# Performance work log

Measured on AMD Instinct MI355X. Metric: run time of the kernel, lower is better.

The kernel has to match this reference:

```python
import jax, jax.numpy as jnp
import numpy as np

B, LQ, LK, D = 32, 1024, 1024, 256

def setup_inputs() -> dict:
    key = jax.random.key(0)
    ks = jax.random.split(key, 7)
    return {
        "raw_query": jax.random.normal(ks[0], (B, LQ, D), dtype=jnp.float32),
        "raw_key": jax.random.normal(ks[1], (B, LK, D), dtype=jnp.float32),
        "raw_value": jax.random.normal(ks[2], (B, LK, D), dtype=jnp.float32),
        "value_mask": jax.random.randint(ks[3], (B, LQ), 0, 2, dtype=jnp.int32),
        "WQ": jax.random.normal(ks[4], (D, D), dtype=jnp.float32) * 0.05,
        "WK": jax.random.normal(ks[5], (D, D), dtype=jnp.float32) * 0.05,
        "WV": jax.random.normal(ks[6], (D, D), dtype=jnp.float32) * 0.05,
    }

def reference(raw_query, raw_key, raw_value, value_mask, WQ, WK, WV):
    # Projections: [B, L, D] @ [D, D]
    Q = raw_query @ WQ
    K = raw_key @ WK
    V = raw_value @ WV
    # Scores: [B, LQ, LK] (use_scale=False -> no 1/sqrt(d_k))
    att = jnp.einsum("bqd,bkd->bqk", Q, K)
    # Mask expanded on axis=2 -> zeroes entire query rows of scores (faithful to tf.where+zeros_like)
    att = jnp.where(value_mask[:, :, None] > 0, att, jnp.zeros((), dtype=att.dtype))
    att = jax.nn.softmax(att, axis=-1)
    # Output: [B, LQ, D]
    return jnp.einsum("bqk,bkd->bqd", att, V)
```

## Files before the change

kernel.cpp:

```cpp
#include <hip/hip_runtime.h>
#include <hip/hip_bf16.h>
#include <math.h>

#define B_ 32
#define L_ 1024
#define D_ 256

typedef _Float16 half8 __attribute__((ext_vector_type(8)));
typedef __fp16   fp16x2 __attribute__((ext_vector_type(2)));
typedef short    s16x8 __attribute__((ext_vector_type(8)));
typedef float    f32x4 __attribute__((ext_vector_type(4)));

typedef __attribute__((address_space(3))) unsigned int lds_u32;
typedef __attribute__((address_space(1))) unsigned int gbl_u32;

__device__ __forceinline__ void gl_lds16(const void* g, void* l) {
    __builtin_amdgcn_global_load_lds((gbl_u32*)g, (lds_u32*)l, 16, 0, 0);
}

__device__ __forceinline__ unsigned short f2bf(float x) {
    unsigned u = __float_as_uint(x);
    u += 0x7FFFu + ((u >> 16) & 1u);
    return (unsigned short)(u >> 16);
}

__device__ __forceinline__ unsigned short f2h(float x) {
    _Float16 h = (_Float16)x;
    unsigned short u;
    __builtin_memcpy(&u, &h, 2);
    return u;
}

__device__ __forceinline__ unsigned pkrtz(float a, float b) {
    fp16x2 v = __builtin_amdgcn_cvt_pkrtz(a, b);
    unsigned u;
    __builtin_memcpy(&u, &v, 4);
    return u;
}

__global__ __launch_bounds__(256) void wprep_kernel(
    const float* __restrict__ W0, const float* __restrict__ W1,
    const float* __restrict__ W2, unsigned short* __restrict__ Wt)
{
    const int z = blockIdx.z;
    const float* __restrict__ W = (z == 0) ? W0 : (z == 1) ? W1 : W2;
    __shared__ unsigned short T[64][72];
    const int k0 = blockIdx.x << 6, n0 = blockIdx.y << 6;
    const int t = threadIdx.x;
    const int r = t >> 2, c0 = (t & 3) << 4;
    #pragma unroll
    for (int j = 0; j < 16; j += 4) {
        float4 w4 = *(const float4*)(W + (size_t)(k0 + r) * 256 + n0 + c0 + j);
        T[c0 + j + 0][r] = f2h(w4.x);
        T[c0 + j + 1][r] = f2h(w4.y);
        T[c0 + j + 2][r] = f2h(w4.z);
        T[c0 + j + 3][r] = f2h(w4.w);
    }
    __syncthreads();
    const int n = t >> 2, kc = (t & 3) << 4;
    unsigned short* dst = Wt + ((size_t)z << 16) + (size_t)(n0 + n) * 256 + k0 + kc;
    *(uint4*)(dst + 0) = *(const uint4*)&T[n][kc + 0];
    *(uint4*)(dst + 8) = *(const uint4*)&T[n][kc + 8];
}

__global__ __launch_bounds__(256) void proj_mfma_kernel(
    const float* __restrict__ A0, const float* __restrict__ A1,
    const float* __restrict__ A2, const unsigned short* __restrict__ Wt,
    unsigned short* __restrict__ Qh, unsigned short* __restrict__ Kh,
    unsigned short* __restrict__ Vt)
{
    __shared__ unsigned short SMEM[32768];
    unsigned short* Asm = SMEM;
    unsigned short* Bsm = SMEM + 16384;

    const int z = blockIdx.z;
    const float* __restrict__ A = (z == 0) ? A0 : (z == 1) ? A1 : A2;
    const int bm = blockIdx.x << 7, bn = blockIdx.y << 7;
    const int t = threadIdx.x, lane = t & 63, w = t >> 6;
    const int wm = (w >> 1) << 6, wn = (w & 1) << 6;

    const float* __restrict__ Ag = A + (size_t)bm * 256;
    const unsigned short* __restrict__ Bg = Wt + ((size_t)z << 16) + (size_t)bn * 256;

    f32x4 acc[4][4];
    const f32x4 z4 = {0.f, 0.f, 0.f, 0.f};
    #pragma unroll
    for (int mi = 0; mi < 4; ++mi)
        #pragma unroll
        for (int ni = 0; ni < 4; ++ni) acc[mi][ni] = z4;

    float4 a_reg[8];

    auto loadA = [&](int it) {
        #pragma unroll
        for (int i = 0; i < 8; ++i) {
            int r  = (t >> 4) + (i << 4);
            int c4 = t & 15;
            a_reg[i] = *(const float4*)(Ag + (size_t)r * 256 + (it << 6) + (c4 << 2));
        }
    };
    auto writeA = [&](int buf) {
        #pragma unroll
        for (int i = 0; i < 8; ++i) {
            int r  = (t >> 4) + (i << 4);
            int c4 = t & 15;
            unsigned h01 = pkrtz(a_reg[i].x, a_reg[i].y);
            unsigned h23 = pkrtz(a_reg[i].z, a_reg[i].w);
            int cs = (c4 >> 1) ^ (r & 7);
            uint2 d2; d2.x = h01; d2.y = h23;
            *(uint2*)&Asm[(buf << 13) + (r << 6) + (cs << 3) + ((c4 & 1) << 2)] = d2;
        }
    };
    auto stageB = [&](int buf, int it) {
        #pragma unroll
        for (int rr = 0; rr < 4; ++rr) {
            int o = (rr << 8) + t;
            int r = o >> 3, c = o & 7;
            int cs = c ^ (r & 7);
            gl_lds16(Bg + (size_t)r * 256 + (it << 6) + (cs << 3),
                     &Bsm[(buf << 13) + (o << 3)]);
        }
    };
    auto compute = [&](int buf) {
        #pragma unroll
        for (int kc = 0; kc < 2; ++kc) {
            half8 af[4], bfr[4];
            #pragma unroll
            for (int mi = 0; mi < 4; ++mi) {
                int m = wm + (mi << 4) + (lane & 15);
                int cs = ((kc << 2) + (lane >> 4)) ^ (m & 7);
                af[mi] = *(const half8*)&Asm[(buf << 13) + (m << 6) + (cs << 3)];
            }
            #pragma unroll
            for (int ni = 0; ni < 4; ++ni) {
                int n = wn + (ni << 4) + (lane & 15);
                int cs = ((kc << 2) + (lane >> 4)) ^ (n & 7);
                bfr[ni] = *(const half8*)&Bsm[(buf << 13) + (n << 6) + (cs << 3)];
            }
            #pragma unroll
            for (int mi = 0; mi < 4; ++mi)
                #pragma unroll
                for (int ni = 0; ni < 4; ++ni)
                    acc[mi][ni] = __builtin_amdgcn_mfma_f32_16x16x32_f16(
                        af[mi], bfr[ni], acc[mi][ni], 0, 0, 0);
        }
    };

    loadA(0);
    writeA(0);
    stageB(0, 0);
    loadA(1);
    __syncthreads();

    for (int it = 0; it < 4; ++it) {
        const int buf = it & 1;
        if (it < 3) {
            stageB(buf ^ 1, it + 1);
            writeA(buf ^ 1);
            if (it < 2) loadA(it + 2);
        }
        compute(buf);
        __syncthreads();
    }

    if (z < 2) {
        unsigned short* __restrict__ C = (z == 0) ? Qh : Kh;
        #pragma unroll
        for (int mi = 0; mi < 4; ++mi) {
            int q = bm + wm + (mi << 4) + ((lane >> 4) << 2);
            #pragma unroll
            for (int ni = 0; ni < 4; ++ni) {
                int col = bn + wn + (ni << 4) + (lane & 15);
                #pragma unroll
                for (int r = 0; r < 4; ++r)
                    C[(size_t)(q + r) * 256 + col] = f2h(acc[mi][ni][r]);
            }
        }
    } else {
        __syncthreads();
        unsigned short (*Tt)[144] = (unsigned short(*)[144])SMEM;
        #pragma unroll
        for (int mi = 0; mi < 4; ++mi) {
            #pragma unroll
            for (int ni = 0; ni < 4; ++ni) {
                int n  = wn + (ni << 4) + (lane & 15);
                int m0 = wm + (mi << 4) + ((lane >> 4) << 2);
                ushort4 v;
                v.x = f2bf(acc[mi][ni][0]);
                v.y = f2bf(acc[mi][ni][1]);
                v.z = f2bf(acc[mi][ni][2]);
                v.w = f2bf(acc[mi][ni][3]);
                *(ushort4*)&Tt[n][m0] = v;
            }
        }
        __syncthreads();
        const int bb = bm >> 10, kin = bm & 1023;
        const int dr = t >> 1, cb = (t & 1) << 6;
        unsigned short* dst = Vt + ((size_t)bb * 256 + bn + dr) * 1024 + kin + cb;
        #pragma unroll
        for (int j = 0; j < 8; ++j)
            *(uint4*)(dst + (j << 3)) = *(const uint4*)&Tt[dr][cb + (j << 3)];
    }
}

__global__ __launch_bounds__(512, 4) void fused_attn_kernel(
    const unsigned short* __restrict__ Qh, const unsigned short* __restrict__ Kh,
    const unsigned short* __restrict__ Vt, const int* __restrict__ mask,
    float* __restrict__ Out)
{
    __shared__ unsigned short Ks[16384];
    __shared__ unsigned short Vs[16384];
    __shared__ unsigned short Ps[64 * 72];
    __shared__ float lred[64][2];

    const int f  = blockIdx.x;
    const int b  = (f & 7) + ((f >> 7) << 3);
    const int q0 = ((f >> 3) & 15) << 6;
    const size_t bL = (size_t)b * L_;
    const int t = threadIdx.x, lane = t & 63, w = t >> 6;
    const int wm_s = (w >> 1) << 4, wn_s = (w & 1) << 5;
    const int wm_v = (w >> 2) << 5, wn_v = (w & 3) << 6;

    const unsigned short* __restrict__ Kb = Kh + (bL << 8);
    const unsigned short* __restrict__ Vb = Vt + (bL << 8);

    auto stageK = [&](int kt) {
        #pragma unroll
        for (int i = 0; i < 4; ++i) {
            int o = (i << 9) + t;
            int r = o >> 5, c = o & 31;
            int cs = (c & 24) | ((c & 7) ^ (r & 7));
            gl_lds16(Kb + (size_t)((kt << 6) + r) * 256 + (cs << 3), &Ks[o << 3]);
        }
    };
    auto stageV = [&](int kt) {
        #pragma unroll
        for (int i = 0; i < 4; ++i) {
            int o = (i << 9) + t;
            int d = o >> 3, c = o & 7;
            int cs = c ^ (d & 7);
            gl_lds16(Vb + ((size_t)d << 10) + (kt << 6) + (cs << 3), &Vs[o << 3]);
        }
    };

    stageK(0);
    stageV(0);

    half8 qf[8];
    {
        int m = wm_s + (lane & 15);
        const unsigned short* qp = Qh + ((bL + q0 + m) << 8) + ((lane >> 4) << 3);
        #pragma unroll
        for (int kc = 0; kc < 8; ++kc)
            qf[kc] = *(const half8*)(qp + (kc << 5));
    }
    int mv[4];
    {
        int qrow = wm_s + ((lane >> 4) << 2);
        #pragma unroll
        for (int r = 0; r < 4; ++r) mv[r] = mask[bL + q0 + qrow + r];
    }

    f32x4 o_acc[2][4];
    const f32x4 z4 = {0.f, 0.f, 0.f, 0.f};
    #pragma unroll
    for (int mi = 0; mi < 2; ++mi)
        #pragma unroll
        for (int ni = 0; ni < 4; ++ni) o_acc[mi][ni] = z4;
    float lacc[4] = {};

    __syncthreads();

    for (int kt = 0; kt < 16; ++kt) {
        if (kt > 0) stageV(kt);

        f32x4 accs[2];
        accs[0] = z4; accs[1] = z4;
        #pragma unroll
        for (int kc = 0; kc < 8; ++kc) {
            int kb = (kc >> 1) << 6, cc = ((kc & 1) << 2) + (lane >> 4);
            int n0 = wn_s + (lane & 15);
            int n1 = n0 + 16;
            half8 bf0 = *(const half8*)&Ks[(n0 << 8) + kb + ((cc ^ (n0 & 7)) << 3)];
            half8 bf1 = *(const half8*)&Ks[(n1 << 8) + kb + ((cc ^ (n1 & 7)) << 3)];
            accs[0] = __builtin_amdgcn_mfma_f32_16x16x32_f16(qf[kc], bf0, accs[0], 0, 0, 0);
            accs[1] = __builtin_amdgcn_mfma_f32_16x16x32_f16(qf[kc], bf1, accs[1], 0, 0, 0);
        }

        {
            int qrow = wm_s + ((lane >> 4) << 2);
            #pragma unroll
            for (int ni = 0; ni < 2; ++ni) {
                int kl = wn_s + (ni << 4) + (lane & 15);
                #pragma unroll
                for (int r = 0; r < 4; ++r) {
                    float p = mv[r] ? __expf(accs[ni][r]) : 1.0f;
                    Ps[(qrow + r) * 72 + kl] = f2bf(p);
                    lacc[r] += p;
                }
            }
        }
        __syncthreads();

        if (kt < 15) stageK(kt + 1);

        #pragma unroll
        for (int kc2 = 0; kc2 < 2; ++kc2) {
            s16x8 pa[2], vb[4];
            #pragma unroll
            for (int mi = 0; mi < 2; ++mi) {
                int m = wm_v + (mi << 4) + (lane & 15);
                pa[mi] = *(const s16x8*)&Ps[m * 72 + (kc2 << 5) + ((lane >> 4) << 3)];
            }
            #pragma unroll
            for (int ni = 0; ni < 4; ++ni) {
                int n = wn_v + (ni << 4) + (lane & 15);
                int cc = (kc2 << 2) + (lane >> 4);
                vb[ni] = *(const s16x8*)&Vs[(n << 6) + ((cc ^ (n & 7)) << 3)];
            }
            #pragma unroll
            for (int mi = 0; mi < 2; ++mi)
                #pragma unroll
                for (int ni = 0; ni < 4; ++ni)
                    o_acc[mi][ni] = __builtin_amdgcn_mfma_f32_16x16x32_bf16(
                        pa[mi], vb[ni], o_acc[mi][ni], 0, 0, 0);
        }
        __syncthreads();
    }

    #pragma unroll
    for (int r = 0; r < 4; ++r) {
        float v = lacc[r];
        v += __shfl_xor(v, 1);
        v += __shfl_xor(v, 2);
        v += __shfl_xor(v, 4);
        v += __shfl_xor(v, 8);
        if ((lane & 15) == 0)
            lred[wm_s + ((lane >> 4) << 2) + r][w & 1] = v;
    }
    __syncthreads();

    #pragma unroll
    for (int mi = 0; mi < 2; ++mi) {
        #pragma unroll
        for (int rr = 0; rr < 4; ++rr) {
            int q = wm_v + (mi << 4) + ((lane >> 4) << 2) + rr;
            float inv = 1.0f / (lred[q][0] + lred[q][1]);
            #pragma unroll
            for (int ni = 0; ni < 4; ++ni) {
                int d = wn_v + (ni << 4) + (lane & 15);
                Out[((bL + q0 + q) << 8) + d] = o_acc[mi][ni][rr] * inv;
            }
        }
    }
}

extern "C" void kernel_launch(void* const* d_in, const int* in_sizes, int n_in,
                              void* d_out, int out_size, void* d_ws, size_t ws_size,
                              hipStream_t stream) {
    const float* rq = (const float*)d_in[0];
    const float* rk = (const float*)d_in[1];
    const float* rv = (const float*)d_in[2];
    const int*   vm = (const int*)d_in[3];
    const float* WQ = (const float*)d_in[4];
    const float* WK = (const float*)d_in[5];
    const float* WV = (const float*)d_in[6];
    float* out = (float*)d_out;

    char* ws = (char*)d_ws;
    unsigned short* Qh = (unsigned short*)(ws);
    unsigned short* Kh = (unsigned short*)(ws + ((size_t)16 << 20));
    unsigned short* Vt = (unsigned short*)(ws + ((size_t)32 << 20));
    unsigned short* Wt = (unsigned short*)(ws + ((size_t)48 << 20));

    dim3 wg(4, 4, 3);
    wprep_kernel<<<wg, 256, 0, stream>>>(WQ, WK, WV, Wt);

    dim3 pg(256, 2, 3);
    proj_mfma_kernel<<<pg, 256, 0, stream>>>(rq, rk, rv, Wt, Qh, Kh, Vt);

    fused_attn_kernel<<<512, 512, 0, stream>>>(Qh, Kh, Vt, vm, out);
}
```

Baseline: 100.6 us.

## Double-buffer K/V tiles and use 128-row query blocks with 1024 threads

Each attention workgroup now handles 128 query rows with 1024 threads, so the grid halves to 256 blocks. K and V tiles are double-buffered in LDS: the next tile is prefetched while the current one is consumed, to hide global load latency and let each staged K/V tile serve twice as many query rows. The probability tile gets an XOR-swizzled layout instead of padding, and its buffer is reused for the row-sum reduction. The cost is about 144KB of LDS and one large block per CU, and the launch bounds of (1024, 4) may squeeze the register budget and cause spills.

```diff
diff --git a/kernel.cpp b/kernel.cpp
--- a/kernel.cpp
+++ b/kernel.cpp
@@ -203,19 +203,19 @@
     }
 }
 
-__global__ __launch_bounds__(512, 4) void fused_attn_kernel(
+__global__ __launch_bounds__(1024, 4) void fused_attn_kernel(
     const unsigned short* __restrict__ Qh, const unsigned short* __restrict__ Kh,
     const unsigned short* __restrict__ Vt, const int* __restrict__ mask,
     float* __restrict__ Out)
 {
-    __shared__ unsigned short Ks[16384];
-    __shared__ unsigned short Vs[16384];
-    __shared__ unsigned short Ps[64 * 72];
-    __shared__ float lred[64][2];
+    __shared__ unsigned short Ks[2][16384];
+    __shared__ unsigned short Vs[2][16384];
+    __shared__ unsigned short Ps[128 * 64];
+    float* lredp = (float*)Ps;
 
     const int f  = blockIdx.x;
-    const int b  = (f & 7) + ((f >> 7) << 3);
-    const int q0 = ((f >> 3) & 15) << 6;
+    const int b  = (f & 7) + ((f >> 6) << 3);
+    const int q0 = ((f >> 3) & 7) << 7;
     const size_t bL = (size_t)b * L_;
     const int t = threadIdx.x, lane = t & 63, w = t >> 6;
     const int wm_s = (w >> 1) << 4, wn_s = (w & 1) << 5;
@@ -224,27 +224,27 @@
     const unsigned short* __restrict__ Kb = Kh + (bL << 8);
     const unsigned short* __restrict__ Vb = Vt + (bL << 8);
 
-    auto stageK = [&](int kt) {
-        #pragma unroll
-        for (int i = 0; i < 4; ++i) {
-            int o = (i << 9) + t;
+    auto stageK = [&](int buf, int kt) {
+        #pragma unroll
+        for (int i = 0; i < 2; ++i) {
+            int o = (i << 10) + t;
             int r = o >> 5, c = o & 31;
             int cs = (c & 24) | ((c & 7) ^ (r & 7));
-            gl_lds16(Kb + (size_t)((kt << 6) + r) * 256 + (cs << 3), &Ks[o << 3]);
-        }
-    };
-    auto stageV = [&](int kt) {
-        #pragma unroll
-        for (int i = 0; i < 4; ++i) {
-            int o = (i << 9) + t;
+            gl_lds16(Kb + (size_t)((kt << 6) + r) * 256 + (cs << 3), &Ks[buf][o << 3]);
+        }
+    };
+    auto stageV = [&](int buf, int kt) {
+        #pragma unroll
+        for (int i = 0; i < 2; ++i) {
+            int o = (i << 10) + t;
             int d = o >> 3, c = o & 7;
             int cs = c ^ (d & 7);
-            gl_lds16(Vb + ((size_t)d << 10) + (kt << 6) + (cs << 3), &Vs[o << 3]);
-        }
-    };
-
-    stageK(0);
-    stageV(0);
+            gl_lds16(Vb + ((size_t)d << 10) + (kt << 6) + (cs << 3), &Vs[buf][o << 3]);
+        }
+    };
+
+    stageK(0, 0);
+    stageV(0, 0);
 
     half8 qf[8];
     {
@@ -272,7 +272,8 @@
     __syncthreads();
 
     for (int kt = 0; kt < 16; ++kt) {
-        if (kt > 0) stageV(kt);
+        const int cur = kt & 1;
+        if (kt < 15) stageV(cur ^ 1, kt + 1);
 
         f32x4 accs[2];
         accs[0] = z4; accs[1] = z4;
@@ -281,8 +282,8 @@
             int kb = (kc >> 1) << 6, cc = ((kc & 1) << 2) + (lane >> 4);
             int n0 = wn_s + (lane & 15);
             int n1 = n0 + 16;
-            half8 bf0 = *(const half8*)&Ks[(n0 << 8) + kb + ((cc ^ (n0 & 7)) << 3)];
-            half8 bf1 = *(const half8*)&Ks[(n1 << 8) + kb + ((cc ^ (n1 & 7)) << 3)];
+            half8 bf0 = *(const half8*)&Ks[cur][(n0 << 8) + kb + ((cc ^ (n0 & 7)) << 3)];
+            half8 bf1 = *(const half8*)&Ks[cur][(n1 << 8) + kb + ((cc ^ (n1 & 7)) << 3)];
             accs[0] = __builtin_amdgcn_mfma_f32_16x16x32_f16(qf[kc], bf0, accs[0], 0, 0, 0);
             accs[1] = __builtin_amdgcn_mfma_f32_16x16x32_f16(qf[kc], bf1, accs[1], 0, 0, 0);
         }
@@ -294,29 +295,30 @@
                 int kl = wn_s + (ni << 4) + (lane & 15);
                 #pragma unroll
                 for (int r = 0; r < 4; ++r) {
+                    int q = qrow + r;
                     float p = mv[r] ? __expf(accs[ni][r]) : 1.0f;
-                    Ps[(qrow + r) * 72 + kl] = f2bf(p);
+                    Ps[(q << 6) + ((((kl >> 3) ^ (q & 7)) << 3)) + (kl & 7)] = f2bf(p);
                     lacc[r] += p;
                 }
             }
         }
         __syncthreads();
 
-        if (kt < 15) stageK(kt + 1);
+        if (kt < 15) stageK(cur ^ 1, kt + 1);
 
         #pragma unroll
         for (int kc2 = 0; kc2 < 2; ++kc2) {
             s16x8 pa[2], vb[4];
+            int cc = (kc2 << 2) + (lane >> 4);
             #pragma unroll
             for (int mi = 0; mi < 2; ++mi) {
                 int m = wm_v + (mi << 4) + (lane & 15);
-                pa[mi] = *(const s16x8*)&Ps[m * 72 + (kc2 << 5) + ((lane >> 4) << 3)];
+                pa[mi] = *(const s16x8*)&Ps[(m << 6) + ((cc ^ (m & 7)) << 3)];
             }
             #pragma unroll
             for (int ni = 0; ni < 4; ++ni) {
                 int n = wn_v + (ni << 4) + (lane & 15);
-                int cc = (kc2 << 2) + (lane >> 4);
-                vb[ni] = *(const s16x8*)&Vs[(n << 6) + ((cc ^ (n & 7)) << 3)];
+                vb[ni] = *(const s16x8*)&Vs[cur][(n << 6) + ((cc ^ (n & 7)) << 3)];
             }
             #pragma unroll
             for (int mi = 0; mi < 2; ++mi)
@@ -336,7 +338,7 @@
         v += __shfl_xor(v, 4);
         v += __shfl_xor(v, 8);
         if ((lane & 15) == 0)
-            lred[wm_s + ((lane >> 4) << 2) + r][w & 1] = v;
+            lredp[((wm_s + ((lane >> 4) << 2) + r) << 1) + (w & 1)] = v;
     }
     __syncthreads();
 
@@ -345,7 +347,7 @@
         #pragma unroll
         for (int rr = 0; rr < 4; ++rr) {
             int q = wm_v + (mi << 4) + ((lane >> 4) << 2) + rr;
-            float inv = 1.0f / (lred[q][0] + lred[q][1]);
+            float inv = 1.0f / (lredp[q << 1] + lredp[(q << 1) + 1]);
             #pragma unroll
             for (int ni = 0; ni < 4; ++ni) {
                 int d = wn_v + (ni << 4) + (lane & 15);
@@ -379,5 +381,5 @@
     dim3 pg(256, 2, 3);
     proj_mfma_kernel<<<pg, 256, 0, stream>>>(rq, rk, rv, Wt, Qh, Kh, Vt);
 
-    fused_attn_kernel<<<512, 512, 0, stream>>>(Qh, Kh, Vt, vm, out);
-}
+    fused_attn_kernel<<<256, 1024, 0, stream>>>(Qh, Kh, Vt, vm, out);
+}
```

Result: faster. 91.51 us (-9.1%).
